# Kernel tuning notes

Measured on AMD Instinct MI355X. Metric: run time of the kernel, lower is better.

Reference implementation:

```python
import jax, jax.numpy as jnp
import numpy as np

K = 5  # local attention kernel size


def layer_norm(x, g, b, eps=1e-3):
    m = jnp.mean(x, axis=-1, keepdims=True)
    v = jnp.var(x, axis=-1, keepdims=True)
    return (x - m) * jax.lax.rsqrt(v + eps) * g + b


def conv1x1(x, w, b):
    return jnp.einsum('bhwc,cd->bhwd', x, w) + b


def nearest_up(x, sh, sw):
    return jnp.repeat(jnp.repeat(x, sh, axis=1), sw, axis=2)


def extract_patches(x, k):
    # tf.image.extract_patches SAME, stride 1: zero pad k//2, gather kxk windows
    # output [B, H, W, k*k, C] with window offsets in row-major order
    p = k // 2
    xp = jnp.pad(x, ((0, 0), (p, p), (p, p), (0, 0)))
    H, W = x.shape[1], x.shape[2]
    pats = [xp[:, i:i + H, j:j + W, :] for i in range(k) for j in range(k)]
    return jnp.stack(pats, axis=3)


def local_attention(query, key, value, k):
    B, qh, qw, cq = query.shape
    _, kh, kw, _ = key.shape
    cv = value.shape[-1]
    hs, ws = qh // kh, qw // kw
    q = query.reshape(B, kh, hs, kw, ws, cq)
    kp = extract_patches(key, k)    # [B, kh, kw, k^2, cq]
    vp = extract_patches(value, k)  # [B, kh, kw, k^2, cv]
    att = jnp.einsum('ijklmn,ijlon->ijklmo', q, kp)  # [B,kh,hs,kw,ws,k^2]
    att = jax.nn.softmax(att, axis=-1)
    out = jnp.einsum('ijklmn,ijlno->ijklmo', att, vp)
    return out.reshape(B, qh, qw, cv)


def setup_inputs() -> dict:
    key = jax.random.key(0)
    ks = jax.random.split(key, 8)
    B, Hf, Wf, Cf = 4, 128, 128, 256
    Hc, Wc, Cc = 64, 64, 512
    E, F = 64, 256
    s = lambda n: 1.0 / np.sqrt(n)
    return {
        'fine': jax.random.normal(ks[0], (B, Hf, Wf, Cf), jnp.float32),
        'coarse': jax.random.normal(ks[1], (B, Hc, Wc, Cc), jnp.float32),
        'ln_f_g': jnp.ones((Cf,), jnp.float32),
        'ln_f_b': jnp.zeros((Cf,), jnp.float32),
        'ln_c_g': jnp.ones((Cc,), jnp.float32),
        'ln_c_b': jnp.zeros((Cc,), jnp.float32),
        'w_gate': jax.random.normal(ks[2], (Cc, 1), jnp.float32) * s(Cc),
        'b_gate': jnp.zeros((1,), jnp.float32),
        'w_qf': jax.random.normal(ks[3], (Cf, E), jnp.float32) * s(Cf),
        'b_qf': jnp.zeros((E,), jnp.float32),
        'w_qc': jax.random.normal(ks[4], (Cc, E), jnp.float32) * s(Cc),
        'b_qc': jnp.zeros((E,), jnp.float32),
        'w_k': jax.random.normal(ks[5], (Cc, E), jnp.float32) * s(Cc),
        'b_k': jnp.zeros((E,), jnp.float32),
        'w_v': jax.random.normal(ks[6], (Cc, F), jnp.float32) * s(Cc),
        'b_v': jnp.zeros((F,), jnp.float32),
    }


def reference(fine, coarse, ln_f_g, ln_f_b, ln_c_g, ln_c_b, w_gate, b_gate,
              w_qf, b_qf, w_qc, b_qc, w_k, b_k, w_v, b_v):
    fine_n = layer_norm(fine, ln_f_g, ln_f_b)
    coarse_n = layer_norm(coarse, ln_c_g, ln_c_b)
    sh = fine.shape[1] // coarse.shape[1]
    sw = fine.shape[2] // coarse.shape[2]
    gate = jax.nn.sigmoid(conv1x1(coarse_n, w_gate, b_gate))
    gate = nearest_up(gate, sh, sw)  # [B, Hf, Wf, 1]
    coarse_up = nearest_up(coarse_n, sh, sw)
    query = conv1x1(fine_n, w_qf, b_qf) * gate + conv1x1(coarse_up, w_qc, b_qc) * (1.0 - gate)
    key = conv1x1(coarse_n, w_k, b_k)
    value = conv1x1(coarse_n, w_v, b_v)
    return local_attention(query, key, value, K)
```

## Files before the change

### kernel.cpp

```cpp
#include <hip/hip_runtime.h>
#include <math.h>

typedef __bf16 bf16x8 __attribute__((ext_vector_type(8)));
typedef float  f32x4  __attribute__((ext_vector_type(4)));
typedef float  vf4    __attribute__((ext_vector_type(4)));

__device__ __forceinline__ float wave_sum(float v) {
#pragma unroll
    for (int m = 1; m < 64; m <<= 1) v += __shfl_xor(v, m, 64);
    return v;
}

__device__ __forceinline__ unsigned short f2bf(float f) {
    union { float f; unsigned int u; } x; x.f = f;
    unsigned int u = x.u;
    u += 0x7fffu + ((u >> 16) & 1u);
    return (unsigned short)(u >> 16);
}
__device__ __forceinline__ float bf2f(unsigned short h) {
    union { unsigned int u; float f; } x; x.u = ((unsigned int)h) << 16;
    return x.f;
}

__device__ __forceinline__ float4 ntload4(const float* p) {
    const vf4 v = __builtin_nontemporal_load((const vf4*)p);
    return make_float4(v.x, v.y, v.z, v.w);
}

__global__ __launch_bounds__(256) void k_wconv(
    const float* __restrict__ w_qc, const float* __restrict__ w_k,
    const float* __restrict__ w_v, const float* __restrict__ w_qf,
    unsigned short* __restrict__ WfragC_hi, unsigned short* __restrict__ WfragC_lo,
    unsigned short* __restrict__ WfragQ_hi, unsigned short* __restrict__ WfragQ_lo)
{
    const int t = blockIdx.x * 256 + threadIdx.x;
    if (t < 24576) {
        const int lane = t & 63, kk = (t >> 6) & 15, nf = t >> 10;
        const int n  = nf * 16 + (lane & 15);
        const int k0 = kk * 32 + (lane >> 4) * 8;
        const float* src; int col, w;
        if (n < 64)       { src = w_qc; col = n;       w = 64;  }
        else if (n < 128) { src = w_k;  col = n - 64;  w = 64;  }
        else              { src = w_v;  col = n - 128; w = 256; }
        unsigned hi[4], lo[4];
#pragma unroll
        for (int i = 0; i < 4; ++i) {
            const float v0 = src[(size_t)(k0 + 2*i)     * w + col];
            const float v1 = src[(size_t)(k0 + 2*i + 1) * w + col];
            const unsigned short h0 = f2bf(v0), h1 = f2bf(v1);
            hi[i] = (unsigned)h0 | ((unsigned)h1 << 16);
            lo[i] = (unsigned)f2bf(v0 - bf2f(h0)) | ((unsigned)f2bf(v1 - bf2f(h1)) << 16);
        }
        *(uint4*)&WfragC_hi[(size_t)t * 8] = *(const uint4*)hi;
        if (nf < 8) *(uint4*)&WfragC_lo[(size_t)t * 8] = *(const uint4*)lo;
    } else if (t < 24576 + 2048) {
        const int t2 = t - 24576;
        const int lane = t2 & 63, kk = (t2 >> 6) & 7, nf = t2 >> 9;
        const int n  = nf * 16 + (lane & 15);
        const int k0 = kk * 32 + (lane >> 4) * 8;
        unsigned hi[4], lo[4];
#pragma unroll
        for (int i = 0; i < 4; ++i) {
            const float v0 = w_qf[(size_t)(k0 + 2*i)     * 64 + n];
            const float v1 = w_qf[(size_t)(k0 + 2*i + 1) * 64 + n];
            const unsigned short h0 = f2bf(v0), h1 = f2bf(v1);
            hi[i] = (unsigned)h0 | ((unsigned)h1 << 16);
            lo[i] = (unsigned)f2bf(v0 - bf2f(h0)) | ((unsigned)f2bf(v1 - bf2f(h1)) << 16);
        }
        *(uint4*)&WfragQ_hi[(size_t)t2 * 8] = *(const uint4*)hi;
        *(uint4*)&WfragQ_lo[(size_t)t2 * 8] = *(const uint4*)lo;
    }
}

#define AP 520
__global__ __launch_bounds__(512) void k_coarse_fused(
    const float* __restrict__ coarse,
    const float* __restrict__ ln_g, const float* __restrict__ ln_b,
    const float* __restrict__ w_gate, const float* __restrict__ b_gate,
    const unsigned short* __restrict__ WfragC_hi,
    const unsigned short* __restrict__ WfragC_lo,
    const float* __restrict__ b_qc, const float* __restrict__ b_k,
    const float* __restrict__ b_v,
    float* __restrict__ gate_o, float* __restrict__ qc_o,
    float* __restrict__ key_o, float* __restrict__ val_o)
{
    __shared__ unsigned short Ah[32 * AP];
    __shared__ unsigned short Al[32 * AP];
    const int tid = threadIdx.x;
    const int lane = tid & 63, wave = tid >> 6;
    const int ci0 = blockIdx.x << 5;

    for (int pp = 0; pp < 4; ++pp) {
        const int p = (wave << 2) + pp;
        const float* src = coarse + (size_t)(ci0 + p) * 512;
        const int c0 = lane * 4, c1 = 256 + lane * 4;
        const float4 x0 = ntload4(src + c0);
        const float4 x1 = ntload4(src + c1);
        float s = (x0.x + x0.y) + (x0.z + x0.w) + (x1.x + x1.y) + (x1.z + x1.w);
        float sq = x0.x*x0.x + x0.y*x0.y + x0.z*x0.z + x0.w*x0.w
                 + x1.x*x1.x + x1.y*x1.y + x1.z*x1.z + x1.w*x1.w;
        s = wave_sum(s); sq = wave_sum(sq);
        const float mean = s * (1.0f / 512.0f);
        const float var  = sq * (1.0f / 512.0f) - mean * mean;
        const float inv  = rsqrtf(var + 1e-3f);
        const float4 g0 = *(const float4*)(ln_g + c0), g1 = *(const float4*)(ln_g + c1);
        const float4 h0 = *(const float4*)(ln_b + c0), h1 = *(const float4*)(ln_b + c1);
        float y[8];
        y[0] = (x0.x - mean) * inv * g0.x + h0.x;
        y[1] = (x0.y - mean) * inv * g0.y + h0.y;
        y[2] = (x0.z - mean) * inv * g0.z + h0.z;
        y[3] = (x0.w - mean) * inv * g0.w + h0.w;
        y[4] = (x1.x - mean) * inv * g1.x + h1.x;
        y[5] = (x1.y - mean) * inv * g1.y + h1.y;
        y[6] = (x1.z - mean) * inv * g1.z + h1.z;
        y[7] = (x1.w - mean) * inv * g1.w + h1.w;
        unsigned short* ah = Ah + p * AP;
        unsigned short* al = Al + p * AP;
#pragma unroll
        for (int j = 0; j < 8; ++j) {
            const int c = (j < 4) ? (c0 + j) : (c1 + j - 4);
            const unsigned short h = f2bf(y[j]);
            ah[c] = h;
            al[c] = f2bf(y[j] - bf2f(h));
        }
        const float4 wg0 = *(const float4*)(w_gate + c0), wg1 = *(const float4*)(w_gate + c1);
        float gd = y[0]*wg0.x + y[1]*wg0.y + y[2]*wg0.z + y[3]*wg0.w
                 + y[4]*wg1.x + y[5]*wg1.y + y[6]*wg1.z + y[7]*wg1.w;
        gd = wave_sum(gd);
        if (lane == 0) gate_o[ci0 + p] = 1.0f / (1.0f + __expf(-(gd + b_gate[0])));
    }
    __syncthreads();

    const int lrow = lane & 15, m16 = lane & 15, lk = (lane >> 4) * 8;
    f32x4 acc_s[2], acc_v[2][2];
#pragma unroll
    for (int i = 0; i < 2; ++i) {
        acc_s[i] = (f32x4){0.f, 0.f, 0.f, 0.f};
        acc_v[i][0] = (f32x4){0.f, 0.f, 0.f, 0.f};
        acc_v[i][1] = (f32x4){0.f, 0.f, 0.f, 0.f};
    }

    const unsigned short* Fs_h = WfragC_hi + ((size_t)(wave * 16) * 64 + lane) * 8;
    const unsigned short* Fs_l = WfragC_lo + ((size_t)(wave * 16) * 64 + lane) * 8;
    const unsigned short* Fv0  = WfragC_hi + ((size_t)((8 + 2*wave) * 16) * 64 + lane) * 8;
    const unsigned short* Fv1  = WfragC_hi + ((size_t)((9 + 2*wave) * 16) * 64 + lane) * 8;
    const int KSTEP = 64 * 8;

    bf16x8 pbh[4], pbl[4], pv0[4], pv1[4];
#pragma unroll
    for (int i = 0; i < 4; ++i) {
        pbh[i] = *(const bf16x8*)(Fs_h + i * KSTEP);
        pbl[i] = *(const bf16x8*)(Fs_l + i * KSTEP);
        pv0[i] = *(const bf16x8*)(Fv0 + i * KSTEP);
        pv1[i] = *(const bf16x8*)(Fv1 + i * KSTEP);
    }

#pragma unroll
    for (int kk = 0; kk < 16; ++kk) {
        const int cur = kk & 3;
        const bf16x8 bh = pbh[cur], bl = pbl[cur], v0 = pv0[cur], v1 = pv1[cur];
        if (kk < 12) {
            pbh[cur] = *(const bf16x8*)(Fs_h + (kk + 4) * KSTEP);
            pbl[cur] = *(const bf16x8*)(Fs_l + (kk + 4) * KSTEP);
            pv0[cur] = *(const bf16x8*)(Fv0 + (kk + 4) * KSTEP);
            pv1[cur] = *(const bf16x8*)(Fv1 + (kk + 4) * KSTEP);
        }
        bf16x8 ah[2], alo[2];
#pragma unroll
        for (int mf = 0; mf < 2; ++mf) {
            ah[mf]  = *(const bf16x8*)&Ah[(mf * 16 + lrow) * AP + kk * 32 + lk];
            alo[mf] = *(const bf16x8*)&Al[(mf * 16 + lrow) * AP + kk * 32 + lk];
        }
#pragma unroll
        for (int mf = 0; mf < 2; ++mf) {
            acc_s[mf] = __builtin_amdgcn_mfma_f32_16x16x32_bf16(ah[mf],  bh, acc_s[mf], 0, 0, 0);
            acc_s[mf] = __builtin_amdgcn_mfma_f32_16x16x32_bf16(alo[mf], bh, acc_s[mf], 0, 0, 0);
            acc_s[mf] = __builtin_amdgcn_mfma_f32_16x16x32_bf16(ah[mf],  bl, acc_s[mf], 0, 0, 0);
            acc_v[mf][0] = __builtin_amdgcn_mfma_f32_16x16x32_bf16(ah[mf], v0, acc_v[mf][0], 0, 0, 0);
            acc_v[mf][1] = __builtin_amdgcn_mfma_f32_16x16x32_bf16(ah[mf], v1, acc_v[mf][1], 0, 0, 0);
        }
    }

    const int rbase = (lane >> 4) * 4;
    const int ns = wave * 16 + m16;
#pragma unroll
    for (int mf = 0; mf < 2; ++mf) {
#pragma unroll
        for (int r = 0; r < 4; ++r) {
            const int m = mf * 16 + rbase + r;
            const int ci = ci0 + m;
            const float vs = acc_s[mf][r];
            if (ns < 64) qc_o [(size_t)ci * 64 + ns]      = vs + b_qc[ns];
            else         key_o[(size_t)ci * 64 + ns - 64] = vs + b_k[ns - 64];
#pragma unroll
            for (int vv = 0; vv < 2; ++vv) {
                const int ch = wave * 32 + vv * 16 + m16;
                val_o[(size_t)ci * 256 + ch] = acc_v[mf][vv][r] + b_v[ch];
            }
        }
    }
}

#define QP 264
__global__ __launch_bounds__(256) void k_query_fused(
    const float* __restrict__ fine,
    const float* __restrict__ ln_g, const float* __restrict__ ln_b,
    const unsigned short* __restrict__ WfragQ_hi,
    const unsigned short* __restrict__ WfragQ_lo,
    const float* __restrict__ b_qf,
    const float* __restrict__ gate_i, const float* __restrict__ qc_i,
    float* __restrict__ query_o)
{
    __shared__ unsigned short Ah[32 * QP];
    __shared__ unsigned short Al[32 * QP];
    const int tid = threadIdx.x;
    const int lane = tid & 63, wave = tid >> 6;
    const int fp0 = blockIdx.x << 5;

    for (int pp = 0; pp < 8; ++pp) {
        const int p = (wave << 3) + pp;
        const float* src = fine + (size_t)(fp0 + p) * 256;
        const int c0 = lane * 4;
        const float4 x = ntload4(src + c0);
        float s = (x.x + x.y) + (x.z + x.w);
        float sq = x.x*x.x + x.y*x.y + x.z*x.z + x.w*x.w;
        s = wave_sum(s); sq = wave_sum(sq);
        const float mean = s * (1.0f / 256.0f);
        const float var  = sq * (1.0f / 256.0f) - mean * mean;
        const float inv  = rsqrtf(var + 1e-3f);
        const float4 g = *(const float4*)(ln_g + c0);
        const float4 h = *(const float4*)(ln_b + c0);
        float y[4];
        y[0] = (x.x - mean) * inv * g.x + h.x;
        y[1] = (x.y - mean) * inv * g.y + h.y;
        y[2] = (x.z - mean) * inv * g.z + h.z;
        y[3] = (x.w - mean) * inv * g.w + h.w;
        unsigned short* ah = Ah + p * QP;
        unsigned short* al = Al + p * QP;
#pragma unroll
        for (int j = 0; j < 4; ++j) {
            const unsigned short hh = f2bf(y[j]);
            ah[c0 + j] = hh;
            al[c0 + j] = f2bf(y[j] - bf2f(hh));
        }
    }
    __syncthreads();

    const int lrow = lane & 15, lk = (lane >> 4) * 8;
    f32x4 acc[2];
    acc[0] = (f32x4){0.f, 0.f, 0.f, 0.f};
    acc[1] = (f32x4){0.f, 0.f, 0.f, 0.f};

    const unsigned short* Fh = WfragQ_hi + ((size_t)(wave * 8) * 64 + lane) * 8;
    const unsigned short* Fl = WfragQ_lo + ((size_t)(wave * 8) * 64 + lane) * 8;
    const int KSTEP = 64 * 8;
    bf16x8 pbh[4], pbl[4];
#pragma unroll
    for (int i = 0; i < 4; ++i) {
        pbh[i] = *(const bf16x8*)(Fh + i * KSTEP);
        pbl[i] = *(const bf16x8*)(Fl + i * KSTEP);
    }

#pragma unroll
    for (int kk = 0; kk < 8; ++kk) {
        const int cur = kk & 3;
        const bf16x8 bh = pbh[cur], bl = pbl[cur];
        if (kk < 4) {
            pbh[cur] = *(const bf16x8*)(Fh + (kk + 4) * KSTEP);
            pbl[cur] = *(const bf16x8*)(Fl + (kk + 4) * KSTEP);
        }
#pragma unroll
        for (int mf = 0; mf < 2; ++mf) {
            const bf16x8 ah = *(const bf16x8*)&Ah[(mf * 16 + lrow) * QP + kk * 32 + lk];
            const bf16x8 al = *(const bf16x8*)&Al[(mf * 16 + lrow) * QP + kk * 32 + lk];
            acc[mf] = __builtin_amdgcn_mfma_f32_16x16x32_bf16(ah, bh, acc[mf], 0, 0, 0);
            acc[mf] = __builtin_amdgcn_mfma_f32_16x16x32_bf16(al, bh, acc[mf], 0, 0, 0);
            acc[mf] = __builtin_amdgcn_mfma_f32_16x16x32_bf16(ah, bl, acc[mf], 0, 0, 0);
        }
    }

    const int n = wave * 16 + (lane & 15);
    const float bias = b_qf[n];
    const int rbase = (lane >> 4) * 4;
#pragma unroll
    for (int mf = 0; mf < 2; ++mf) {
#pragma unroll
        for (int r = 0; r < 4; ++r) {
            const int m = mf * 16 + rbase + r;
            const int fp = fp0 + m;
            const int wx = fp & 127, h = (fp >> 7) & 127, b2 = fp >> 14;
            const int ci = ((b2 << 6) + (h >> 1)) * 64 + (wx >> 1);
            const float gt = gate_i[ci];
            const float qcv = qc_i[(size_t)ci * 64 + n];
            query_o[(size_t)fp * 64 + n] = (acc[mf][r] + bias) * gt + qcv * (1.0f - gt);
        }
    }
}

#define LDS_K_HI 0
#define LDS_K_LO 4096
#define LDS_VT   8192
#define LDS_ATT  26624
__global__ __launch_bounds__(256) void k_attn_mfma(
    const float* __restrict__ query, const float* __restrict__ key,
    const float* __restrict__ value, float* __restrict__ out)
{
    __shared__ unsigned short LDS[30720];
    const int tid = threadIdx.x;
    const int lane = tid & 63, wave = tid >> 6;
    const int m16 = lane & 15, g4 = lane >> 4;
    const int blk = blockIdx.x;
    const int bx = blk & 15, by = (blk >> 4) & 15, bb = blk >> 8;
    const int cy0 = by << 2, cx0 = bx << 2;

    {
        const int tau = lane;
        const int chunk = wave;
        const int cy = cy0 - 2 + (tau >> 3), cx = cx0 - 2 + (tau & 7);
        float v[16];
        if ((unsigned)cy < 64u && (unsigned)cx < 64u) {
            const float* src = key + ((size_t)(((bb << 6) + cy) << 6) + cx) * 64 + chunk * 16;
#pragma unroll
            for (int i = 0; i < 4; ++i) {
                const float4 x = *(const float4*)(src + i * 4);
                v[i*4+0]=x.x; v[i*4+1]=x.y; v[i*4+2]=x.z; v[i*4+3]=x.w;
            }
        } else {
#pragma unroll
            for (int i = 0; i < 16; ++i) v[i] = 0.f;
        }
        unsigned hi[8] __attribute__((aligned(16)));
        unsigned lo[8] __attribute__((aligned(16)));
#pragma unroll
        for (int i = 0; i < 8; ++i) {
            const unsigned short h0 = f2bf(v[2*i]), h1 = f2bf(v[2*i+1]);
            hi[i] = (unsigned)h0 | ((unsigned)h1 << 16);
            const unsigned short l0 = f2bf(v[2*i] - bf2f(h0));
            const unsigned short l1 = f2bf(v[2*i+1] - bf2f(h1));
            lo[i] = (unsigned)l0 | ((unsigned)l1 << 16);
        }
#pragma unroll
        for (int g = 0; g < 2; ++g) {
            const int G = chunk * 2 + g;
            const int a = tau * 64 + ((G ^ (tau & 7)) * 8);
            *(uint4*)&LDS[LDS_K_HI + a] = *(const uint4*)&hi[g*4];
            *(uint4*)&LDS[LDS_K_LO + a] = *(const uint4*)&lo[g*4];
        }
    }

    {
        const int p2 = lane & 31;
        const int pos0 = p2 * 2;
        const int cy = cy0 - 2 + (pos0 >> 3);
        const int cx = cx0 - 2 + (pos0 & 7);
        const bool ok0 = ((unsigned)cy < 64u) && ((unsigned)cx < 64u);
        const bool ok1 = ((unsigned)cy < 64u) && ((unsigned)(cx + 1) < 64u);
        const size_t base0 = ((size_t)(((bb << 6) + cy) << 6) + cx) * 256;
        const int chbase = wave * 64 + (lane >> 5) * 4;
#pragma unroll
        for (int it = 0; it < 8; ++it) {
            const int ch = chbase + it * 8;
            const float4 a = ok0 ? *(const float4*)(value + base0 + ch)
                                 : make_float4(0.f, 0.f, 0.f, 0.f);
            const float4 b = ok1 ? *(const float4*)(value + base0 + 256 + ch)
                                 : make_float4(0.f, 0.f, 0.f, 0.f);
            const float av[4] = {a.x, a.y, a.z, a.w};
            const float bv[4] = {b.x, b.y, b.z, b.w};
#pragma unroll
            for (int i = 0; i < 4; ++i) {
                const unsigned w = (unsigned)f2bf(av[i]) | ((unsigned)f2bf(bv[i]) << 16);
                *(unsigned*)&LDS[LDS_VT + (ch + i) * 72 + pos0] = w;
            }
        }
    }

    {
        const uint4 z = {0u, 0u, 0u, 0u};
        *(uint4*)&LDS[LDS_ATT + tid * 8] = z;
        *(uint4*)&LDS[LDS_ATT + 2048 + tid * 8] = z;
    }

    const int fybase = (by << 3) + (wave << 1);
    bf16x8 qh[2], ql[2];
    {
        const int fy = fybase + (m16 >> 3);
        const int fx = (bx << 3) + (m16 & 7);
        const float* qsrc = query + ((size_t)(((bb << 7) + fy) << 7) + fx) * 64;
#pragma unroll
        for (int kf = 0; kf < 2; ++kf) {
            float q8[8];
#pragma unroll
            for (int i = 0; i < 2; ++i) {
                const float4 x = *(const float4*)(qsrc + kf * 32 + g4 * 8 + i * 4);
                q8[i*4+0]=x.x; q8[i*4+1]=x.y; q8[i*4+2]=x.z; q8[i*4+3]=x.w;
            }
            union { unsigned u[4]; bf16x8 b; } uh, ul;
#pragma unroll
            for (int i = 0; i < 4; ++i) {
                const unsigned short h0 = f2bf(q8[2*i]), h1 = f2bf(q8[2*i+1]);
                uh.u[i] = (unsigned)h0 | ((unsigned)h1 << 16);
                const unsigned short l0 = f2bf(q8[2*i] - bf2f(h0));
                const unsigned short l1 = f2bf(q8[2*i+1] - bf2f(h1));
                ul.u[i] = (unsigned)l0 | ((unsigned)l1 << 16);
            }
            qh[kf] = uh.b; ql[kf] = ul.b;
        }
    }

    __syncthreads();

    f32x4 sc[3];
#pragma unroll
    for (int nf = 0; nf < 3; ++nf) sc[nf] = (f32x4){0.f, 0.f, 0.f, 0.f};
#pragma unroll
    for (int nf = 0; nf < 3; ++nf) {
        const int row = 8 * wave + nf * 16 + m16;
#pragma unroll
        for (int kf = 0; kf < 2; ++kf) {
            const int G = kf * 4 + g4;
            const int a = row * 64 + ((G ^ (m16 & 7)) * 8);
            const bf16x8 bh = *(const bf16x8*)&LDS[LDS_K_HI + a];
            const bf16x8 bl = *(const bf16x8*)&LDS[LDS_K_LO + a];
            sc[nf] = __builtin_amdgcn_mfma_f32_16x16x32_bf16(qh[kf], bh, sc[nf], 0, 0, 0);
            sc[nf] = __builtin_amdgcn_mfma_f32_16x16x32_bf16(ql[kf], bh, sc[nf], 0, 0, 0);
            sc[nf] = __builtin_amdgcn_mfma_f32_16x16x32_bf16(qh[kf], bl, sc[nf], 0, 0, 0);
        }
    }

    float e[3][4];
    float rinv[4];
#pragma unroll
    for (int r = 0; r < 4; ++r) {
        const int m = 4 * g4 + r;
        const int j = (m & 7) >> 1;
        float mr = -1e30f;
#pragma unroll
        for (int nf = 0; nf < 3; ++nf) {
            const int tf = nf * 16 + m16;
            const int tc = tf & 7;
            const bool c = (tf < 40) && (tc >= j) && (tc <= j + 4);
            e[nf][r] = c ? sc[nf][r] : -1e30f;
            mr = fmaxf(mr, e[nf][r]);
        }
#pragma unroll
        for (int msk = 1; msk < 16; msk <<= 1) mr = fmaxf(mr, __shfl_xor(mr, msk, 64));
        float s = 0.f;
#pragma unroll
        for (int nf = 0; nf < 3; ++nf) {
            const float ev = (e[nf][r] > -1e29f) ? __expf(e[nf][r] - mr) : 0.f;
            e[nf][r] = ev; s += ev;
        }
#pragma unroll
        for (int msk = 1; msk < 16; msk <<= 1) s += __shfl_xor(s, msk, 64);
        rinv[r] = 1.0f / s;
    }

#pragma unroll
    for (int nf = 0; nf < 3; ++nf) {
        const int t = 8 * wave + nf * 16 + m16;
        if (t < 64) {
#pragma unroll
            for (int r = 0; r < 4; ++r) {
                const int prow = wave * 16 + 4 * g4 + r;
                const int a = prow * 64 + (((t >> 3) ^ (prow & 7)) * 8) + (t & 7);
                LDS[LDS_ATT + a] = f2bf(e[nf][r] * rinv[r]);
            }
        }
    }

    bf16x8 af[2];
#pragma unroll
    for (int kf = 0; kf < 2; ++kf) {
        const int row = wave * 16 + m16;
        const int G = kf * 4 + g4;
        af[kf] = *(const bf16x8*)&LDS[LDS_ATT + row * 64 + ((G ^ (m16 & 7)) * 8)];
    }
    f32x4 ao[16];
#pragma unroll
    for (int nf = 0; nf < 16; ++nf) ao[nf] = (f32x4){0.f, 0.f, 0.f, 0.f};
#pragma unroll
    for (int nf = 0; nf < 16; ++nf) {
        const int ch = nf * 16 + m16;
#pragma unroll
        for (int kf = 0; kf < 2; ++kf) {
            const bf16x8 b = *(const bf16x8*)&LDS[LDS_VT + ch * 72 + kf * 32 + g4 * 8];
            ao[nf] = __builtin_amdgcn_mfma_f32_16x16x32_bf16(af[kf], b, ao[nf], 0, 0, 0);
        }
    }

#pragma unroll
    for (int r = 0; r < 4; ++r) {
        const int m = 4 * g4 + r;
        const int fy = fybase + (m >> 3);
        const int fx = (bx << 3) + (m & 7);
        float* op = out + ((size_t)(((bb << 7) + fy) << 7) + fx) * 256 + m16;
#pragma unroll
        for (int nf = 0; nf < 16; ++nf)
            op[nf * 16] = ao[nf][r];
    }
}

extern "C" void kernel_launch(void* const* d_in, const int* in_sizes, int n_in,
                              void* d_out, int out_size, void* d_ws, size_t ws_size,
                              hipStream_t stream)
{
    const float* fine   = (const float*)d_in[0];
    const float* coarse = (const float*)d_in[1];
    const float* ln_f_g = (const float*)d_in[2];
    const float* ln_f_b = (const float*)d_in[3];
    const float* ln_c_g = (const float*)d_in[4];
    const float* ln_c_b = (const float*)d_in[5];
    const float* w_gate = (const float*)d_in[6];
    const float* b_gate = (const float*)d_in[7];
    const float* w_qf   = (const float*)d_in[8];
    const float* b_qf   = (const float*)d_in[9];
    const float* w_qc   = (const float*)d_in[10];
    const float* b_qc   = (const float*)d_in[11];
    const float* w_k    = (const float*)d_in[12];
    const float* b_k    = (const float*)d_in[13];
    const float* w_v    = (const float*)d_in[14];
    const float* b_v    = (const float*)d_in[15];
    float* out = (float*)d_out;

    float* ws   = (float*)d_ws;
    float* gate = ws;
    float* qc   = gate + 16384;
    float* keyb = qc   + (size_t)16384 * 64;
    float* valb = keyb + (size_t)16384 * 64;
    float* qry  = valb + (size_t)16384 * 256;
    unsigned short* WfragC_hi = (unsigned short*)(qry + (size_t)65536 * 64);
    unsigned short* WfragC_lo = WfragC_hi + (size_t)24576 * 8;
    unsigned short* WfragQ_hi = WfragC_lo + (size_t)8192 * 8;
    unsigned short* WfragQ_lo = WfragQ_hi + (size_t)2048 * 8;

    k_wconv<<<104, 256, 0, stream>>>(w_qc, w_k, w_v, w_qf,
                                     WfragC_hi, WfragC_lo, WfragQ_hi, WfragQ_lo);
    k_coarse_fused<<<512, 512, 0, stream>>>(coarse, ln_c_g, ln_c_b, w_gate, b_gate,
                                            WfragC_hi, WfragC_lo, b_qc, b_k, b_v,
                                            gate, qc, keyb, valb);
    k_query_fused<<<2048, 256, 0, stream>>>(fine, ln_f_g, ln_f_b, WfragQ_hi, WfragQ_lo, b_qf,
                                            gate, qc, qry);
    k_attn_mfma<<<1024, 256, 0, stream>>>(qry, keyb, valb, out);
}
```

Before: 85.84 us.

## Store key/query as packed bf16 hi/lo pairs and value as bf16 in producers

Producer kernels now write key and query as packed bf16 hi/lo split words and value as plain bf16, instead of fp32. The attention kernel reads these directly, so it no longer converts on load and reads half as many bytes for value. The attention block index is also remapped (blk0&7)*128 + (blk0>>3) to change which tiles run next to each other, likely for cache locality. Value was already rounded to bf16 before, so precision is unchanged. The split conversion work moves into the producer epilogues.

```diff
diff --git a/kernel.cpp b/kernel.cpp
--- a/kernel.cpp
+++ b/kernel.cpp
@@ -20,6 +20,11 @@
 __device__ __forceinline__ float bf2f(unsigned short h) {
     union { unsigned int u; float f; } x; x.u = ((unsigned int)h) << 16;
     return x.f;
+}
+__device__ __forceinline__ unsigned packsplit(float v) {
+    const unsigned short h = f2bf(v);
+    const unsigned short l = f2bf(v - bf2f(h));
+    return (unsigned)h | ((unsigned)l << 16);
 }
 
 __device__ __forceinline__ float4 ntload4(const float* p) {
@@ -82,7 +87,7 @@
     const float* __restrict__ b_qc, const float* __restrict__ b_k,
     const float* __restrict__ b_v,
     float* __restrict__ gate_o, float* __restrict__ qc_o,
-    float* __restrict__ key_o, float* __restrict__ val_o)
+    unsigned* __restrict__ key_pk, unsigned short* __restrict__ val_b)
 {
     __shared__ unsigned short Ah[32 * AP];
     __shared__ unsigned short Al[32 * AP];
@@ -190,12 +195,12 @@
             const int m = mf * 16 + rbase + r;
             const int ci = ci0 + m;
             const float vs = acc_s[mf][r];
-            if (ns < 64) qc_o [(size_t)ci * 64 + ns]      = vs + b_qc[ns];
-            else         key_o[(size_t)ci * 64 + ns - 64] = vs + b_k[ns - 64];
+            if (ns < 64) qc_o[(size_t)ci * 64 + ns] = vs + b_qc[ns];
+            else         key_pk[(size_t)ci * 64 + ns - 64] = packsplit(vs + b_k[ns - 64]);
 #pragma unroll
             for (int vv = 0; vv < 2; ++vv) {
                 const int ch = wave * 32 + vv * 16 + m16;
-                val_o[(size_t)ci * 256 + ch] = acc_v[mf][vv][r] + b_v[ch];
+                val_b[(size_t)ci * 256 + ch] = f2bf(acc_v[mf][vv][r] + b_v[ch]);
             }
         }
     }
@@ -209,7 +214,7 @@
     const unsigned short* __restrict__ WfragQ_lo,
     const float* __restrict__ b_qf,
     const float* __restrict__ gate_i, const float* __restrict__ qc_i,
-    float* __restrict__ query_o)
+    unsigned* __restrict__ qry_pk)
 {
     __shared__ unsigned short Ah[32 * QP];
     __shared__ unsigned short Al[32 * QP];
@@ -292,7 +297,7 @@
             const int ci = ((b2 << 6) + (h >> 1)) * 64 + (wx >> 1);
             const float gt = gate_i[ci];
             const float qcv = qc_i[(size_t)ci * 64 + n];
-            query_o[(size_t)fp * 64 + n] = (acc[mf][r] + bias) * gt + qcv * (1.0f - gt);
+            qry_pk[(size_t)fp * 64 + n] = packsplit((acc[mf][r] + bias) * gt + qcv * (1.0f - gt));
         }
     }
 }
@@ -302,49 +307,44 @@
 #define LDS_VT   8192
 #define LDS_ATT  26624
 __global__ __launch_bounds__(256) void k_attn_mfma(
-    const float* __restrict__ query, const float* __restrict__ key,
-    const float* __restrict__ value, float* __restrict__ out)
+    const unsigned* __restrict__ qry_pk, const unsigned* __restrict__ key_pk,
+    const unsigned short* __restrict__ val_b, float* __restrict__ out)
 {
     __shared__ unsigned short LDS[30720];
     const int tid = threadIdx.x;
     const int lane = tid & 63, wave = tid >> 6;
     const int m16 = lane & 15, g4 = lane >> 4;
-    const int blk = blockIdx.x;
+    const int blk0 = blockIdx.x;
+    const int blk = (blk0 & 7) * 128 + (blk0 >> 3);
     const int bx = blk & 15, by = (blk >> 4) & 15, bb = blk >> 8;
     const int cy0 = by << 2, cx0 = bx << 2;
 
     {
-        const int tau = lane;
-        const int chunk = wave;
+        const int tau = lane, chunk = wave;
         const int cy = cy0 - 2 + (tau >> 3), cx = cx0 - 2 + (tau & 7);
-        float v[16];
+        unsigned w[16];
         if ((unsigned)cy < 64u && (unsigned)cx < 64u) {
-            const float* src = key + ((size_t)(((bb << 6) + cy) << 6) + cx) * 64 + chunk * 16;
+            const unsigned* src = key_pk + ((size_t)(((bb << 6) + cy) << 6) + cx) * 64 + chunk * 16;
+#pragma unroll
+            for (int i = 0; i < 4; ++i)
+                *(uint4*)&w[i * 4] = *(const uint4*)(src + i * 4);
+        } else {
+#pragma unroll
+            for (int i = 0; i < 16; ++i) w[i] = 0u;
+        }
+#pragma unroll
+        for (int g = 0; g < 2; ++g) {
+            unsigned hi[4], lo[4];
 #pragma unroll
             for (int i = 0; i < 4; ++i) {
-                const float4 x = *(const float4*)(src + i * 4);
-                v[i*4+0]=x.x; v[i*4+1]=x.y; v[i*4+2]=x.z; v[i*4+3]=x.w;
+                const unsigned w0 = w[g * 8 + 2 * i], w1 = w[g * 8 + 2 * i + 1];
+                hi[i] = (w0 & 0xffffu) | ((w1 & 0xffffu) << 16);
+                lo[i] = (w0 >> 16) | (w1 & 0xffff0000u);
             }
-        } else {
-#pragma unroll
-            for (int i = 0; i < 16; ++i) v[i] = 0.f;
-        }
-        unsigned hi[8] __attribute__((aligned(16)));
-        unsigned lo[8] __attribute__((aligned(16)));
-#pragma unroll
-        for (int i = 0; i < 8; ++i) {
-            const unsigned short h0 = f2bf(v[2*i]), h1 = f2bf(v[2*i+1]);
-            hi[i] = (unsigned)h0 | ((unsigned)h1 << 16);
-            const unsigned short l0 = f2bf(v[2*i] - bf2f(h0));
-            const unsigned short l1 = f2bf(v[2*i+1] - bf2f(h1));
-            lo[i] = (unsigned)l0 | ((unsigned)l1 << 16);
-        }
-#pragma unroll
-        for (int g = 0; g < 2; ++g) {
             const int G = chunk * 2 + g;
             const int a = tau * 64 + ((G ^ (tau & 7)) * 8);
-            *(uint4*)&LDS[LDS_K_HI + a] = *(const uint4*)&hi[g*4];
-            *(uint4*)&LDS[LDS_K_LO + a] = *(const uint4*)&lo[g*4];
+            *(uint4*)&LDS[LDS_K_HI + a] = *(const uint4*)hi;
+            *(uint4*)&LDS[LDS_K_LO + a] = *(const uint4*)lo;
         }
     }
 
@@ -356,20 +356,19 @@
         const bool ok0 = ((unsigned)cy < 64u) && ((unsigned)cx < 64u);
         const bool ok1 = ((unsigned)cy < 64u) && ((unsigned)(cx + 1) < 64u);
         const size_t base0 = ((size_t)(((bb << 6) + cy) << 6) + cx) * 256;
-        const int chbase = wave * 64 + (lane >> 5) * 4;
-#pragma unroll
-        for (int it = 0; it < 8; ++it) {
-            const int ch = chbase + it * 8;
-            const float4 a = ok0 ? *(const float4*)(value + base0 + ch)
-                                 : make_float4(0.f, 0.f, 0.f, 0.f);
-            const float4 b = ok1 ? *(const float4*)(value + base0 + 256 + ch)
-                                 : make_float4(0.f, 0.f, 0.f, 0.f);
-            const float av[4] = {a.x, a.y, a.z, a.w};
-            const float bv[4] = {b.x, b.y, b.z, b.w};
-#pragma unroll
-            for (int i = 0; i < 4; ++i) {
-                const unsigned w = (unsigned)f2bf(av[i]) | ((unsigned)f2bf(bv[i]) << 16);
-                *(unsigned*)&LDS[LDS_VT + (ch + i) * 72 + pos0] = w;
+        const int chbase = wave * 64 + (lane >> 5) * 8;
+        const uint4 z = {0u, 0u, 0u, 0u};
+#pragma unroll
+        for (int it = 0; it < 4; ++it) {
+            const int ch = chbase + it * 16;
+            const uint4 a = ok0 ? *(const uint4*)(val_b + base0 + ch) : z;
+            const uint4 b = ok1 ? *(const uint4*)(val_b + base0 + 256 + ch) : z;
+            const unsigned short* au = (const unsigned short*)&a;
+            const unsigned short* bu = (const unsigned short*)&b;
+#pragma unroll
+            for (int j = 0; j < 8; ++j) {
+                const unsigned w = (unsigned)au[j] | ((unsigned)bu[j] << 16);
+                *(unsigned*)&LDS[LDS_VT + (ch + j) * 72 + pos0] = w;
             }
         }
     }
@@ -385,23 +384,18 @@
     {
         const int fy = fybase + (m16 >> 3);
         const int fx = (bx << 3) + (m16 & 7);
-        const float* qsrc = query + ((size_t)(((bb << 7) + fy) << 7) + fx) * 64;
+        const unsigned* qsrc = qry_pk + ((size_t)(((bb << 7) + fy) << 7) + fx) * 64;
 #pragma unroll
         for (int kf = 0; kf < 2; ++kf) {
-            float q8[8];
-#pragma unroll
-            for (int i = 0; i < 2; ++i) {
-                const float4 x = *(const float4*)(qsrc + kf * 32 + g4 * 8 + i * 4);
-                q8[i*4+0]=x.x; q8[i*4+1]=x.y; q8[i*4+2]=x.z; q8[i*4+3]=x.w;
-            }
+            unsigned w[8];
+            *(uint4*)&w[0] = *(const uint4*)(qsrc + kf * 32 + g4 * 8);
+            *(uint4*)&w[4] = *(const uint4*)(qsrc + kf * 32 + g4 * 8 + 4);
             union { unsigned u[4]; bf16x8 b; } uh, ul;
 #pragma unroll
             for (int i = 0; i < 4; ++i) {
-                const unsigned short h0 = f2bf(q8[2*i]), h1 = f2bf(q8[2*i+1]);
-                uh.u[i] = (unsigned)h0 | ((unsigned)h1 << 16);
-                const unsigned short l0 = f2bf(q8[2*i] - bf2f(h0));
-                const unsigned short l1 = f2bf(q8[2*i+1] - bf2f(h1));
-                ul.u[i] = (unsigned)l0 | ((unsigned)l1 << 16);
+                const unsigned w0 = w[2 * i], w1 = w[2 * i + 1];
+                uh.u[i] = (w0 & 0xffffu) | ((w1 & 0xffffu) << 16);
+                ul.u[i] = (w0 >> 16) | (w1 & 0xffff0000u);
             }
             qh[kf] = uh.b; ql[kf] = ul.b;
         }
@@ -525,10 +519,10 @@
     float* ws   = (float*)d_ws;
     float* gate = ws;
     float* qc   = gate + 16384;
-    float* keyb = qc   + (size_t)16384 * 64;
-    float* valb = keyb + (size_t)16384 * 64;
-    float* qry  = valb + (size_t)16384 * 256;
-    unsigned short* WfragC_hi = (unsigned short*)(qry + (size_t)65536 * 64);
+    unsigned* key_pk = (unsigned*)(qc + (size_t)16384 * 64);
+    unsigned short* val_b = (unsigned short*)(key_pk + (size_t)16384 * 64);
+    unsigned* qry_pk = (unsigned*)(val_b + (size_t)16384 * 256);
+    unsigned short* WfragC_hi = (unsigned short*)(qry_pk + (size_t)65536 * 64);
     unsigned short* WfragC_lo = WfragC_hi + (size_t)24576 * 8;
     unsigned short* WfragQ_hi = WfragC_lo + (size_t)8192 * 8;
     unsigned short* WfragQ_lo = WfragQ_hi + (size_t)2048 * 8;
@@ -537,8 +531,8 @@
                                      WfragC_hi, WfragC_lo, WfragQ_hi, WfragQ_lo);
     k_coarse_fused<<<512, 512, 0, stream>>>(coarse, ln_c_g, ln_c_b, w_gate, b_gate,
                                             WfragC_hi, WfragC_lo, b_qc, b_k, b_v,
-                                            gate, qc, keyb, valb);
+                                            gate, qc, key_pk, val_b);
     k_query_fused<<<2048, 256, 0, stream>>>(fine, ln_f_g, ln_f_b, WfragQ_hi, WfragQ_lo, b_qf,
-                                            gate, qc, qry);
-    k_attn_mfma<<<1024, 256, 0, stream>>>(qry, keyb, valb, out);
-}
+                                            gate, qc, qry_pk);
+    k_attn_mfma<<<1024, 256, 0, stream>>>(qry_pk, key_pk, val_b, out);
+}
```

New measurement: 102.3 us. +19.2%, slower.
